# Performance work log

Measured on AMD Instinct MI355X. Metric: run time of the kernel, lower is better.

Reference implementation:

```python
import jax, jax.numpy as jnp
import numpy as np

B, H, SQ, SKV, D = 2, 16, 2048, 3072, 64
NUM_PT = 1024  # SKV = NUM_PT + SQ


def setup_inputs() -> dict:
    key = jax.random.key(0)
    kq, kk, kv = jax.random.split(key, 3)
    q = jax.random.normal(kq, (B, H, SQ, D), dtype=jnp.float32)
    k = jax.random.normal(kk, (B, H, SKV, D), dtype=jnp.float32)
    v = jax.random.normal(kv, (B, H, SKV, D), dtype=jnp.float32)
    return {"q": q, "k": k, "v": v, "num_pt": NUM_PT}


def _prefix_causal_mask(sq, skv, num_pt):
    # kv_idx < num_pt always visible (global prefix); otherwise causal on
    # shifted index: q_idx >= kv_idx - num_pt
    q_idx = jnp.arange(sq)[:, None]   # [SQ,1]
    kv_idx = jnp.arange(skv)[None, :]  # [1,SKV]
    return (kv_idx < num_pt) | (q_idx >= kv_idx - num_pt)  # [SQ,SKV]


def reference(q, k, v, num_pt):
    scale = 1.0 / jnp.sqrt(jnp.asarray(q.shape[-1], q.dtype))
    # [B,H,SQ,SKV]
    scores = jnp.einsum("bhqd,bhkd->bhqk", q, k) * scale
    mask = _prefix_causal_mask(q.shape[2], k.shape[2], num_pt)  # [SQ,SKV]
    neg = jnp.asarray(jnp.finfo(scores.dtype).min, scores.dtype)
    scores = jnp.where(mask[None, None], scores, neg)
    probs = jax.nn.softmax(scores, axis=-1)
    return jnp.einsum("bhqk,bhkd->bhqd", probs, v)
```

## Files before the change

kernel.cpp:

```cpp
#include <hip/hip_runtime.h>

#define B_ 2
#define H_ 16
#define SQ_ 2048
#define SKV_ 3072
#define DH 64
#define QT 128
#define KVT 64
#define LDK 72

typedef __attribute__((ext_vector_type(4))) float f32x4;
typedef __attribute__((ext_vector_type(8))) short bf16x8;

struct PAset { bf16x8 p00, p01, p10, p11; };

__device__ __forceinline__ unsigned cvt_pk(float a, float b) {
  unsigned r;
  asm("v_cvt_pk_bf16_f32 %0, %1, %2" : "=v"(r) : "v"(a), "v"(b));
  return r;
}
__device__ __forceinline__ void pl16_swap(unsigned& a, unsigned& b) {
  asm("v_permlane16_swap_b32 %0, %1" : "+v"(a), "+v"(b));
}
__device__ __forceinline__ void pl32_swap(unsigned& a, unsigned& b) {
  asm("v_permlane32_swap_b32 %0, %1" : "+v"(a), "+v"(b));
}


#define QKSM(TIDX, KSP, PAS)                                              \
  {                                                                       \
    const int kb = (TIDX)*KVT;                                            \
    f32x4 s0[4], s1[4];                                                   \
    _Pragma("unroll") for (int mg = 0; mg < 4; ++mg) {                    \
      bf16x8 ka0 = *(const bf16x8*)&KSP[mg * 16 + lq][quad * 8];          \
      bf16x8 ka1 = *(const bf16x8*)&KSP[mg * 16 + lq][32 + quad * 8];     \
      f32x4 c0 = (f32x4){0.f, 0.f, 0.f, 0.f};                             \
      f32x4 c1 = (f32x4){0.f, 0.f, 0.f, 0.f};                             \
      c0 = __builtin_amdgcn_mfma_f32_16x16x32_bf16(ka0, qf0[0], c0, 0, 0, 0);\
      c0 = __builtin_amdgcn_mfma_f32_16x16x32_bf16(ka1, qf0[1], c0, 0, 0, 0);\
      c1 = __builtin_amdgcn_mfma_f32_16x16x32_bf16(ka0, qf1[0], c1, 0, 0, 0);\
      c1 = __builtin_amdgcn_mfma_f32_16x16x32_bf16(ka1, qf1[1], c1, 0, 0, 0);\
      s0[mg] = c0; s1[mg] = c1;                                           \
    }                                                                     \
    if (kb + KVT - 1 > q0 + w * 32 + num_pt) {                            \
      _Pragma("unroll") for (int mg = 0; mg < 4; ++mg)                    \
        _Pragma("unroll") for (int r = 0; r < 4; ++r)                     \
          if (kb + mg * 16 + quad * 4 + r > lim0) s0[mg][r] = -__builtin_inff();\
    }                                                                     \
    if (kb + KVT - 1 > q0 + w * 32 + 16 + num_pt) {                       \
      _Pragma("unroll") for (int mg = 0; mg < 4; ++mg)                    \
        _Pragma("unroll") for (int r = 0; r < 4; ++r)                     \
          if (kb + mg * 16 + quad * 4 + r > lim1) s1[mg][r] = -__builtin_inff();\
    }                                                                     \
    _Pragma("unroll") for (int mg = 0; mg < 4; ++mg)                      \
      _Pragma("unroll") for (int r = 0; r < 4; ++r) {                     \
        float p0 = __builtin_amdgcn_exp2f(s0[mg][r]);                     \
        float p1 = __builtin_amdgcn_exp2f(s1[mg][r]);                     \
        s0[mg][r] = p0; l40[r] += p0;                                     \
        s1[mg][r] = p1; l41[r] += p1;                                     \
      }                                                                   \
    {                                                                     \
      unsigned U[4], W[4];                                                \
      _Pragma("unroll") for (int mg = 0; mg < 4; ++mg) {                  \
        U[mg] = cvt_pk(s0[mg][0], s0[mg][1]);                             \
        W[mg] = cvt_pk(s0[mg][2], s0[mg][3]);                             \
      }                                                                   \
      pl32_swap(U[0], U[1]); pl16_swap(U[0], U[1]);                       \
      pl32_swap(W[0], W[1]); pl16_swap(W[0], W[1]);                       \
      pl32_swap(U[2], U[3]); pl16_swap(U[2], U[3]);                       \
      pl32_swap(W[2], W[3]); pl16_swap(W[2], W[3]);                       \
      union { unsigned u[4]; bf16x8 h; } t0, t1;                          \
      t0.u[0] = U[0]; t0.u[1] = W[0]; t0.u[2] = U[1]; t0.u[3] = W[1];     \
      t1.u[0] = U[2]; t1.u[1] = W[2]; t1.u[2] = U[3]; t1.u[3] = W[3];     \
      PAS.p00 = t0.h; PAS.p01 = t1.h;                                     \
    }                                                                     \
    {                                                                     \
      unsigned U[4], W[4];                                                \
      _Pragma("unroll") for (int mg = 0; mg < 4; ++mg) {                  \
        U[mg] = cvt_pk(s1[mg][0], s1[mg][1]);                             \
        W[mg] = cvt_pk(s1[mg][2], s1[mg][3]);                             \
      }                                                                   \
      pl32_swap(U[0], U[1]); pl16_swap(U[0], U[1]);                       \
      pl32_swap(W[0], W[1]); pl16_swap(W[0], W[1]);                       \
      pl32_swap(U[2], U[3]); pl16_swap(U[2], U[3]);                       \
      pl32_swap(W[2], W[3]); pl16_swap(W[2], W[3]);                       \
      union { unsigned u[4]; bf16x8 h; } t0, t1;                          \
      t0.u[0] = U[0]; t0.u[1] = W[0]; t0.u[2] = U[1]; t0.u[3] = W[1];     \
      t1.u[0] = U[2]; t1.u[1] = W[2]; t1.u[2] = U[3]; t1.u[3] = W[3];     \
      PAS.p10 = t0.h; PAS.p11 = t1.h;                                     \
    }                                                                     \
  }

#define PVACC(VTP, PAS)                                                   \
  {                                                                       \
    _Pragma("unroll") for (int dg = 0; dg < 4; ++dg) {                    \
      bf16x8 vb0 = *(const bf16x8*)&VTP[dg * 16 + lq][quad * 8];          \
      bf16x8 vb1 = *(const bf16x8*)&VTP[dg * 16 + lq][32 + quad * 8];     \
      O0[dg] = __builtin_amdgcn_mfma_f32_16x16x32_bf16(vb0, PAS.p00, O0[dg], 0, 0, 0);\
      O0[dg] = __builtin_amdgcn_mfma_f32_16x16x32_bf16(vb1, PAS.p01, O0[dg], 0, 0, 0);\
      O1[dg] = __builtin_amdgcn_mfma_f32_16x16x32_bf16(vb0, PAS.p10, O1[dg], 0, 0, 0);\
      O1[dg] = __builtin_amdgcn_mfma_f32_16x16x32_bf16(vb1, PAS.p11, O1[dg], 0, 0, 0);\
    }                                                                     \
  }

#define STAGE(RK, RV, KW, VW)                                             \
  {                                                                       \
    union { unsigned u[4]; bf16x8 hh; } ta, tb;                           \
    ta.u[0] = cvt_pk(RK[0].x, RK[0].y);                                   \
    ta.u[1] = cvt_pk(RK[0].z, RK[0].w);                                   \
    ta.u[2] = cvt_pk(RK[1].x, RK[1].y);                                   \
    ta.u[3] = cvt_pk(RK[1].z, RK[1].w);                                   \
    *(bf16x8*)&KW[krow][kc] = ta.hh;                                      \
    tb.u[0] = cvt_pk(RK[2].x, RK[2].y);                                   \
    tb.u[1] = cvt_pk(RK[2].z, RK[2].w);                                   \
    tb.u[2] = cvt_pk(RK[3].x, RK[3].y);                                   \
    tb.u[3] = cvt_pk(RK[3].z, RK[3].w);                                   \
    *(bf16x8*)&KW[krow][kc + 8] = tb.hh;                                  \
    *(unsigned*)&VW[vd0 + 0][2 * vp] = cvt_pk(RV[0].x, RV[2].x);          \
    *(unsigned*)&VW[vd0 + 1][2 * vp] = cvt_pk(RV[0].y, RV[2].y);          \
    *(unsigned*)&VW[vd0 + 2][2 * vp] = cvt_pk(RV[0].z, RV[2].z);          \
    *(unsigned*)&VW[vd0 + 3][2 * vp] = cvt_pk(RV[0].w, RV[2].w);          \
    *(unsigned*)&VW[vd0 + 4][2 * vp] = cvt_pk(RV[1].x, RV[3].x);          \
    *(unsigned*)&VW[vd0 + 5][2 * vp] = cvt_pk(RV[1].y, RV[3].y);          \
    *(unsigned*)&VW[vd0 + 6][2 * vp] = cvt_pk(RV[1].z, RV[3].z);          \
    *(unsigned*)&VW[vd0 + 7][2 * vp] = cvt_pk(RV[1].w, RV[3].w);          \
  }

#define LOADT(PIDX, NK, NV)                                               \
  {                                                                       \
    int pidx = (PIDX);                                                    \
    if (pidx > n_tiles - 1) pidx = n_tiles - 1;                           \
    const size_t nb = (size_t)pidx * KVT * DH;                            \
    NK[0] = *(const float4*)(kQp + nb);                                   \
    NK[1] = *(const float4*)(kQp + nb + 4);                               \
    NK[2] = *(const float4*)(kQp + nb + 8);                               \
    NK[3] = *(const float4*)(kQp + nb + 12);                              \
    NV[0] = *(const float4*)(vQp + nb);                                   \
    NV[1] = *(const float4*)(vQp + nb + 4);                               \
    NV[2] = *(const float4*)(vQp + nb + DH);                              \
    NV[3] = *(const float4*)(vQp + nb + DH + 4);                          \
  }

#define BODY(T, RK, RV, NK, NV, PACUR, PANXT)                             \
  {                                                                       \
    LOADT((T) + 3, NK, NV)                                                \
    STAGE(RK, RV, ksC, vtC)                                               \
    QKSM((T) + 1, ksB, PANXT)                                             \
    PVACC(vtA, PACUR)                                                     \
    __syncthreads();                                                      \
    { short (*tk)[LDK] = ksA; ksA = ksB; ksB = ksC; ksC = tk;             \
      short (*tv)[LDK] = vtA; vtA = vtB; vtB = vtC; vtC = tv; }           \
  }

__global__ __launch_bounds__(256, 2) void attn_fwd(
    const float* __restrict__ qg_, const float* __restrict__ kg_,
    const float* __restrict__ vg_, const int* __restrict__ num_pt_p,
    float* __restrict__ og_) {
  __shared__ __align__(16) short KsAll[3][KVT][LDK];
  __shared__ __align__(16) short VtAll[3][DH][LDK];

  const int tid  = (int)threadIdx.x;
  const int lane = tid & 63;
  const int w    = tid >> 6;
  const int lq   = lane & 15;
  const int quad = lane >> 4;
  const int x    = (int)blockIdx.x;
  const int y    = (int)blockIdx.y;
  const int qb   = (y & 16) ? x : (15 - x);
  const int num_pt = *num_pt_p;
  const int q0   = qb * QT;

  const float* qg = qg_ + (size_t)y * SQ_ * DH;
  const float* kg = kg_ + (size_t)y * SKV_ * DH;
  const float* vg = vg_ + (size_t)y * SKV_ * DH;
  float*       og = og_ + (size_t)y * SQ_ * DH;

  const float SC = 0.125f * 1.44269504088896341f;

  const int qrow0 = q0 + w * 32 + lq;
  const int qrow1 = qrow0 + 16;
  bf16x8 qf0[2], qf1[2];
#pragma unroll
  for (int f = 0; f < 2; ++f) {
    const float* qp = qg + (size_t)(f ? qrow1 : qrow0) * DH + quad * 8;
#pragma unroll
    for (int kh = 0; kh < 2; ++kh) {
      float4 a = *(const float4*)(qp + kh * 32);
      float4 b = *(const float4*)(qp + kh * 32 + 4);
      union { unsigned u[4]; bf16x8 hh; } tq;
      tq.u[0] = cvt_pk(a.x * SC, a.y * SC);
      tq.u[1] = cvt_pk(a.z * SC, a.w * SC);
      tq.u[2] = cvt_pk(b.x * SC, b.y * SC);
      tq.u[3] = cvt_pk(b.z * SC, b.w * SC);
      if (f) qf1[kh] = tq.hh; else qf0[kh] = tq.hh;
    }
  }

  f32x4 O0[4], O1[4];
#pragma unroll
  for (int i = 0; i < 4; ++i) {
    O0[i] = (f32x4){0.f, 0.f, 0.f, 0.f};
    O1[i] = (f32x4){0.f, 0.f, 0.f, 0.f};
  }
  f32x4 l40 = (f32x4){0.f, 0.f, 0.f, 0.f};
  f32x4 l41 = (f32x4){0.f, 0.f, 0.f, 0.f};

  int n_tiles = (q0 + QT - 1 + num_pt) / KVT + 1;
  if (n_tiles > SKV_ / KVT) n_tiles = SKV_ / KVT;

  const int krow = tid >> 2;
  const int kc   = (tid & 3) * 16;
  const int vp   = tid & 31;
  const int vd0  = (tid >> 5) * 8;
  const float* kQp = kg + (size_t)krow * DH + kc;
  const float* vQp = vg + (size_t)(2 * vp) * DH + vd0;

  const int lim0 = qrow0 + num_pt;
  const int lim1 = qrow1 + num_pt;

  short (*ksA)[LDK] = KsAll[0], (*ksB)[LDK] = KsAll[1], (*ksC)[LDK] = KsAll[2];
  short (*vtA)[LDK] = VtAll[0], (*vtB)[LDK] = VtAll[1], (*vtC)[LDK] = VtAll[2];

  float4 Ak[4], Av[4], Bk[4], Bv[4];
  LOADT(0, Ak, Av)
  LOADT(1, Bk, Bv)
  STAGE(Ak, Av, ksA, vtA)
  STAGE(Bk, Bv, ksB, vtB)
  LOADT(2, Bk, Bv)
  __syncthreads();

  PAset paE, paO;
  QKSM(0, ksA, paE)

  const int NB = n_tiles - 1;
  int t = 0;
  for (; t + 1 < NB; t += 2) {
    BODY(t,     Bk, Bv, Ak, Av, paE, paO)
    BODY(t + 1, Ak, Av, Bk, Bv, paO, paE)
  }
  if (t < NB) {
    BODY(t, Bk, Bv, Ak, Av, paE, paO)
    PVACC(vtA, paO)
  } else {
    PVACC(vtA, paE)
  }

  {
    float lr = l40[0] + l40[1] + l40[2] + l40[3];
    lr += __shfl_xor(lr, 16);
    lr += __shfl_xor(lr, 32);
    float inv = 1.0f / lr;
    float* op = og + (size_t)qrow0 * DH + quad * 4;
#pragma unroll
    for (int dg = 0; dg < 4; ++dg) {
      float4 o4;
      o4.x = O0[dg][0] * inv;
      o4.y = O0[dg][1] * inv;
      o4.z = O0[dg][2] * inv;
      o4.w = O0[dg][3] * inv;
      *(float4*)(op + dg * 16) = o4;
    }
  }
  {
    float lr = l41[0] + l41[1] + l41[2] + l41[3];
    lr += __shfl_xor(lr, 16);
    lr += __shfl_xor(lr, 32);
    float inv = 1.0f / lr;
    float* op = og + (size_t)qrow1 * DH + quad * 4;
#pragma unroll
    for (int dg = 0; dg < 4; ++dg) {
      float4 o4;
      o4.x = O1[dg][0] * inv;
      o4.y = O1[dg][1] * inv;
      o4.z = O1[dg][2] * inv;
      o4.w = O1[dg][3] * inv;
      *(float4*)(op + dg * 16) = o4;
    }
  }
}

extern "C" void kernel_launch(void* const* d_in, const int* in_sizes, int n_in,
                              void* d_out, int out_size, void* d_ws, size_t ws_size,
                              hipStream_t stream) {
  const float* q = (const float*)d_in[0];
  const float* k = (const float*)d_in[1];
  const float* v = (const float*)d_in[2];
  const int* np  = (const int*)d_in[3];
  float* out = (float*)d_out;
  dim3 grid(SQ_ / QT, B_ * H_);
  attn_fwd<<<grid, dim3(256), 0, stream>>>(q, k, v, np, out);
}
```

Baseline: 160.2 us.

## Restructure KV pipeline to process tile pairs with four LDS buffers

Replaces the three-buffer software pipeline, where the QK softmax of tile t+1 overlapped the PV of tile t with one barrier per tile, with a four-buffer scheme. Each iteration stages and loads two tiles and computes two tiles back to back, so there is one barrier per two tiles. The aim is to halve the synchronisation count. In exchange it drops the QK/PV interleaving across tiles, raises LDS use, which may affect two-blocks-per-CU occupancy, and adds a more complex tail for leftover tiles.

```diff
diff --git a/kernel.cpp b/kernel.cpp
--- a/kernel.cpp
+++ b/kernel.cpp
@@ -103,6 +103,13 @@
     }                                                                     \
   }
 
+#define TILE1(TIDX, BI)                                                   \
+  {                                                                       \
+    PAset pa;                                                             \
+    QKSM((TIDX), KsAll[BI], pa)                                           \
+    PVACC(VtAll[BI], pa)                                                  \
+  }
+
 #define STAGE(RK, RV, KW, VW)                                             \
   {                                                                       \
     union { unsigned u[4]; bf16x8 hh; } ta, tb;                           \
@@ -141,23 +148,23 @@
     NV[3] = *(const float4*)(vQp + nb + DH + 4);                          \
   }
 
-#define BODY(T, RK, RV, NK, NV, PACUR, PANXT)                             \
-  {                                                                       \
-    LOADT((T) + 3, NK, NV)                                                \
-    STAGE(RK, RV, ksC, vtC)                                               \
-    QKSM((T) + 1, ksB, PANXT)                                             \
-    PVACC(vtA, PACUR)                                                     \
+#define BODYPAIR(T, I0, I1, I2, I3)                                       \
+  {                                                                       \
+    STAGE(Ak, Av, KsAll[I2], VtAll[I2])                                   \
+    STAGE(Bk, Bv, KsAll[I3], VtAll[I3])                                   \
+    LOADT((T) + 4, Ak, Av)                                                \
+    LOADT((T) + 5, Bk, Bv)                                                \
+    TILE1((T), I0)                                                        \
+    TILE1((T) + 1, I1)                                                    \
     __syncthreads();                                                      \
-    { short (*tk)[LDK] = ksA; ksA = ksB; ksB = ksC; ksC = tk;             \
-      short (*tv)[LDK] = vtA; vtA = vtB; vtB = vtC; vtC = tv; }           \
   }
 
 __global__ __launch_bounds__(256, 2) void attn_fwd(
     const float* __restrict__ qg_, const float* __restrict__ kg_,
     const float* __restrict__ vg_, const int* __restrict__ num_pt_p,
     float* __restrict__ og_) {
-  __shared__ __align__(16) short KsAll[3][KVT][LDK];
-  __shared__ __align__(16) short VtAll[3][DH][LDK];
+  __shared__ __align__(16) short KsAll[4][KVT][LDK];
+  __shared__ __align__(16) short VtAll[4][DH][LDK];
 
   const int tid  = (int)threadIdx.x;
   const int lane = tid & 63;
@@ -218,31 +225,28 @@
   const int lim0 = qrow0 + num_pt;
   const int lim1 = qrow1 + num_pt;
 
-  short (*ksA)[LDK] = KsAll[0], (*ksB)[LDK] = KsAll[1], (*ksC)[LDK] = KsAll[2];
-  short (*vtA)[LDK] = VtAll[0], (*vtB)[LDK] = VtAll[1], (*vtC)[LDK] = VtAll[2];
-
   float4 Ak[4], Av[4], Bk[4], Bv[4];
   LOADT(0, Ak, Av)
   LOADT(1, Bk, Bv)
-  STAGE(Ak, Av, ksA, vtA)
-  STAGE(Bk, Bv, ksB, vtB)
-  LOADT(2, Bk, Bv)
+  STAGE(Ak, Av, KsAll[0], VtAll[0])
+  STAGE(Bk, Bv, KsAll[1], VtAll[1])
+  LOADT(2, Ak, Av)
+  LOADT(3, Bk, Bv)
   __syncthreads();
 
-  PAset paE, paO;
-  QKSM(0, ksA, paE)
-
-  const int NB = n_tiles - 1;
   int t = 0;
-  for (; t + 1 < NB; t += 2) {
-    BODY(t,     Bk, Bv, Ak, Av, paE, paO)
-    BODY(t + 1, Ak, Av, Bk, Bv, paO, paE)
-  }
-  if (t < NB) {
-    BODY(t, Bk, Bv, Ak, Av, paE, paO)
-    PVACC(vtA, paO)
-  } else {
-    PVACC(vtA, paE)
+  for (; t + 3 < n_tiles; t += 4) {
+    BODYPAIR(t,     0, 1, 2, 3)
+    BODYPAIR(t + 2, 2, 3, 0, 1)
+  }
+  {
+    const int r = n_tiles - t;
+    if (r == 1) {
+      TILE1(t, 0)
+    } else if (r >= 2) {
+      BODYPAIR(t, 0, 1, 2, 3)
+      if (r == 3) TILE1(t + 2, 2)
+    }
   }
 
   {
```

After: 214.9 us. 34.2% more time.
